# Kernel tuning notes

Measured on AMD Instinct MI355X. Metric: run time of the kernel, lower is better.

The kernel has to match this reference:

```python
import jax, jax.numpy as jnp
import numpy as np

NUM_ITERS = 3

def squash(t, axis):
    # scale = |t|^2/(1+|t|^2); out = scale * t / |t|
    sn = jnp.sum(t * t, axis=axis, keepdims=True)
    return (sn / (1.0 + sn)) * t / jnp.sqrt(sn)


def setup_inputs() -> dict:
    key = jax.random.key(0)
    k1, k2, k3, k4 = jax.random.split(key, 4)
    B = 128
    inputs = jax.random.normal(k1, (B, 256, 20, 20), dtype=jnp.float32)
    conv_w = jax.random.normal(k2, (8, 32, 256, 9, 9), dtype=jnp.float32) * 0.05
    conv_b = jax.random.normal(k3, (8, 32), dtype=jnp.float32) * 0.05
    route_weights = jax.random.normal(k4, (10, 1152, 8, 16), dtype=jnp.float32)
    return {"inputs": inputs, "conv_w": conv_w, "conv_b": conv_b,
            "route_weights": route_weights}


def reference(inputs, conv_w, conv_b, route_weights):
    B = inputs.shape[0]
    K, O, Cin, kh, kw = conv_w.shape          # 8 capsules, 32 out-chans each
    # --- primary capsules: 8 parallel convs fused into one grouped-output conv ---
    w = conv_w.reshape(K * O, Cin, kh, kw)
    out = jax.lax.conv_general_dilated(
        inputs, w, window_strides=(2, 2), padding='VALID',
        dimension_numbers=('NCHW', 'OIHW', 'NCHW'))  # [B, K*O, 6, 6]
    out = out + conv_b.reshape(K * O)[None, :, None, None]
    H = out.shape[-1]
    x = out.reshape(B, K, O * H * H).transpose(0, 2, 1)  # [B, 1152, 8]
    x = squash(x, axis=2)
    # --- routing layer ---
    # prediction_vectors: x[None,:,:,None,:] @ W[:,None,:,:,:] -> [10,B,1152,1,16]
    pred = jnp.einsum('bri,crio->cbro', x, route_weights)[:, :, :, None, :]
    logits = jnp.zeros_like(pred)
    v = None
    for i in range(NUM_ITERS):
        # routing_softmax(dim=2): softmax over the routes axis (faithful to source)
        c = jax.nn.softmax(logits, axis=2)
        s = jnp.sum(c * pred, axis=2, keepdims=True)  # [10,B,1,1,16]
        v = squash(s, axis=1)                          # squash default dim=1 (batch) -- faithful
        if i != NUM_ITERS - 1:
            logits = logits + jnp.sum(pred * v, axis=-1, keepdims=True)
    # [10,B,1,1,16] -> squeeze -> [10,B,16] -> permute(1,0,2) -> [B,10,16]
    return jnp.squeeze(v).transpose(1, 0, 2)
```

## Files before the change

kernel.cpp:

```cpp
#include <hip/hip_runtime.h>
#include <math.h>

typedef _Float16 f16;
typedef _Float16 f16x8 __attribute__((ext_vector_type(8)));
typedef float f32x4 __attribute__((ext_vector_type(4)));
typedef float f32x8 __attribute__((ext_vector_type(8)));

#define AS1 __attribute__((address_space(1)))
#define AS3 __attribute__((address_space(3)))

__device__ __forceinline__ void gld_lds16(const f16* g, f16* l) {
#if defined(__has_builtin) && __has_builtin(__builtin_amdgcn_global_load_lds)
    __builtin_amdgcn_global_load_lds((const AS1 void*)g, (AS3 void*)l, 16, 0, 0);
#else
    *(uint4*)l = *(const uint4*)g;
#endif
}

__global__ __launch_bounds__(256) void transpose_input(
    const float* __restrict__ inp, f16* __restrict__ out)
{
    const int b = blockIdx.x, c0 = blockIdx.y * 32, p0 = blockIdx.z * 32;
    const int tx = threadIdx.x, ty = threadIdx.y;
    __shared__ float t[32][33];
#pragma unroll
    for (int j = 0; j < 4; ++j) {
        int c = ty + j * 8, p = p0 + tx;
        if (p < 400) t[c][tx] = inp[((size_t)b * 256 + c0 + c) * 400 + p];
    }
    __syncthreads();
#pragma unroll
    for (int j = 0; j < 4; ++j) {
        int p = p0 + ty + j * 8;
        if (p < 400) out[((size_t)b * 400 + p) * 256 + c0 + tx] = (f16)t[tx][ty + j * 8];
    }
}

__global__ __launch_bounds__(256) void permute_w(
    const float* __restrict__ cw, f16* __restrict__ w_t)
{
    const int n = blockIdx.x, t = threadIdx.x;
    __shared__ f16 buf[81 * 258];
    const float* src = cw + (size_t)n * 20736;
    for (int i = t; i < 20736; i += 256) {
        int cin = i / 81, p = i - cin * 81;
        buf[p * 258 + cin] = (f16)src[i];
    }
    __syncthreads();
    f16* dst = w_t + (size_t)n * 20736;
    for (int j = t; j < 20736; j += 256) {
        int p = j >> 8, cin = j & 255;
        dst[j] = buf[p * 258 + cin];
    }
}

#define SPLITK 14
__global__ __launch_bounds__(256, 2) void conv_mfma(
    const f16* __restrict__ in_t,
    const f16* __restrict__ w_t,
    f16* __restrict__ part)
{
    __shared__ f16 As[3][128 * 32];
    __shared__ f16 Bs[3][256 * 32];
    const int tid = threadIdx.x;
    const int lane = tid & 63, wave = tid >> 6;
    const int wm = wave >> 1, wn = wave & 1;

    const int bid = blockIdx.x + 36 * blockIdx.z;
    const int wgid = (bid & 7) * 63 + (bid >> 3);
    const int m0 = (wgid % 36) * 128;
    const int kz = wgid / 36;

    const int kc0 = kz * 46 + (kz < 4 ? kz : 4);
    const int NT  = (kz < 4) ? 47 : 46;

    int srcA[2], srcB[4];
#pragma unroll
    for (int i = 0; i < 2; ++i) {
        int pairp = i * 32 + (tid >> 3);
        int chunk8 = (tid & 7) ^ (pairp & 7);
        int e = chunk8 >> 2, q4 = chunk8 & 3;
        int m = m0 + pairp * 2 + e;
        int b = m / 36, hw = m - b * 36;
        int ho = hw / 6, wo = hw - ho * 6;
        srcA[i] = ((b * 20 + 2 * ho) * 20 + 2 * wo) * 256 + q4 * 8;
    }
#pragma unroll
    for (int i = 0; i < 4; ++i) {
        int pairp = i * 32 + (tid >> 3);
        int chunk8 = (tid & 7) ^ (pairp & 7);
        int e = chunk8 >> 2, q4 = chunk8 & 3;
        int n = pairp * 2 + e;
        srcB[i] = n * 20736 + q4 * 8;
    }

    const int row = lane & 15, quad = lane >> 4;
    int offA[4], offB[8];
#pragma unroll
    for (int mt = 0; mt < 4; ++mt) {
        int m = wm * 64 + mt * 16 + row;
        int ph8 = (((m & 1) << 2) + quad) ^ ((m >> 1) & 7);
        offA[mt] = (m >> 1) * 64 + ph8 * 8;
    }
#pragma unroll
    for (int nt = 0; nt < 8; ++nt) {
        int n = wn * 128 + nt * 16 + row;
        int ph8 = (((n & 1) << 2) + quad) ^ ((n >> 1) & 7);
        offB[nt] = (n >> 1) * 64 + ph8 * 8;
    }

    f32x4 acc[4][8] = {};

#define STAGE(T, BUF) do {                                                    \
        int kc = kc0 + (T);                                                   \
        int p = kc >> 3, cq = kc & 7;                                         \
        int kh = p / 9, kw = p - kh * 9;                                      \
        int koffA = (kh * 20 + kw) * 256 + cq * 32;                           \
        int koffB = kc * 32;                                                  \
        _Pragma("unroll")                                                     \
        for (int i = 0; i < 2; ++i)                                           \
            gld_lds16(in_t + srcA[i] + koffA, &As[BUF][i * 2048 + tid * 8]);  \
        _Pragma("unroll")                                                     \
        for (int i = 0; i < 4; ++i)                                           \
            gld_lds16(w_t + srcB[i] + koffB, &Bs[BUF][i * 2048 + tid * 8]);   \
    } while (0)

    STAGE(0, 0);
    STAGE(1, 1);

    int buf = 0;
    for (int t = 0; t < NT; ++t) {
        if (t + 1 < NT)
            asm volatile("s_waitcnt vmcnt(6)\n\ts_barrier" ::: "memory");
        else
            asm volatile("s_waitcnt vmcnt(0)\n\ts_barrier" ::: "memory");
        if (t + 2 < NT) {
            int bn = buf + 2; if (bn >= 3) bn -= 3;
            STAGE(t + 2, bn);
        }
        const f16* Ab = &As[buf][0];
        const f16* Bb = &Bs[buf][0];
        f16x8 af[4], bfr[8];
#pragma unroll
        for (int mt = 0; mt < 4; ++mt) af[mt] = *(const f16x8*)(Ab + offA[mt]);
#pragma unroll
        for (int nt = 0; nt < 8; ++nt) bfr[nt] = *(const f16x8*)(Bb + offB[nt]);
        __builtin_amdgcn_s_setprio(1);
#pragma unroll
        for (int mt = 0; mt < 4; ++mt)
#pragma unroll
            for (int nt = 0; nt < 8; ++nt)
                acc[mt][nt] = __builtin_amdgcn_mfma_f32_16x16x32_f16(
                    af[mt], bfr[nt], acc[mt][nt], 0, 0, 0);
        __builtin_amdgcn_s_setprio(0);
        if (++buf == 3) buf = 0;
    }
#undef STAGE

    const int col = lane & 15, qr = (lane >> 4) * 4;
    f16* pb = part + (size_t)kz * 4608 * 256;
#pragma unroll
    for (int mt = 0; mt < 4; ++mt)
#pragma unroll
        for (int rg = 0; rg < 4; ++rg) {
            int m = m0 + wm * 64 + mt * 16 + qr + rg;
#pragma unroll
            for (int nt = 0; nt < 8; ++nt) {
                int n = wn * 128 + nt * 16 + col;
                pb[(size_t)m * 256 + n] = (f16)acc[mt][nt][rg];
            }
        }
}

__global__ __launch_bounds__(256) void combine_squash(
    const f16* __restrict__ part, const float* __restrict__ bias,
    float* __restrict__ x)
{
    int idx = blockIdx.x * 256 + threadIdx.x;
    int m = idx >> 5, o = idx & 31;
    int b = m / 36, hw = m - b * 36;
    float val[8];
#pragma unroll
    for (int k = 0; k < 8; ++k) val[k] = bias[k * 32 + o];
#pragma unroll
    for (int s = 0; s < SPLITK; ++s) {
        const f16* p = part + ((size_t)s * 4608 + m) * 256 + o;
#pragma unroll
        for (int k = 0; k < 8; ++k) val[k] += (float)p[k * 32];
    }
    float sn = 0.f;
#pragma unroll
    for (int k = 0; k < 8; ++k) sn += val[k] * val[k];
    float scale = sqrtf(sn) / (1.f + sn);
    int r = o * 36 + hw;
    float* xp = x + ((size_t)b * 1152 + r) * 8;
#pragma unroll
    for (int k = 0; k < 8; ++k) xp[k] = val[k] * scale;
}

__global__ __launch_bounds__(256) void pred_s0(
    const float* __restrict__ x, const float* __restrict__ rw,
    f16* __restrict__ pred, float* __restrict__ s0)
{
    const int c = blockIdx.x, r0 = blockIdx.y * 32, b0 = blockIdx.z * 32;
    const int tid = threadIdx.x;
    const int o = tid & 15, rp = tid >> 4;
    const int r = r0 + rp * 2;

    __shared__ float s_sh[32 * 16];
    s_sh[tid] = 0.f; s_sh[tid + 256] = 0.f;

    float W0[8], W1[8];
    const float* wb = rw + ((size_t)(c * 1152 + r) * 8) * 16 + o;
#pragma unroll
    for (int k = 0; k < 8; ++k) { W0[k] = wb[k * 16]; W1[k] = wb[128 + k * 16]; }
    __syncthreads();

    for (int bb = 0; bb < 32; ++bb) {
        const int b = b0 + bb;
        const float4* xp = (const float4*)(x + ((size_t)b * 1152 + r) * 8);
        float4 xa = xp[0], xb = xp[1], xc = xp[2], xd = xp[3];
        float p0 = xa.x * W0[0] + xa.y * W0[1] + xa.z * W0[2] + xa.w * W0[3]
                 + xb.x * W0[4] + xb.y * W0[5] + xb.z * W0[6] + xb.w * W0[7];
        float p1 = xc.x * W1[0] + xc.y * W1[1] + xc.z * W1[2] + xc.w * W1[3]
                 + xd.x * W1[4] + xd.y * W1[5] + xd.z * W1[6] + xd.w * W1[7];
        f16* pb = pred + ((size_t)(c * 128 + b) * 1152 + r) * 16 + o;
        pb[0]  = (f16)p0;
        pb[16] = (f16)p1;
        float ps = p0 + p1;
        ps += __shfl_xor(ps, 16);
        ps += __shfl_xor(ps, 32);
        if ((tid & 63) < 16) atomicAdd(&s_sh[bb * 16 + o], ps);
    }
    __syncthreads();
    for (int i = tid; i < 512; i += 256) {
        int bb = i >> 4, oo = i & 15;
        atomicAdd(&s0[((size_t)c * 128 + b0 + bb) * 16 + oo], s_sh[i]);
    }
}

__global__ __launch_bounds__(256) void route_f16(
    const f16* __restrict__ pred, const float* __restrict__ s_in,
    const float* __restrict__ z_in, const float* __restrict__ a_in,
    float* __restrict__ a_out, float* __restrict__ s_out, float* __restrict__ z_out)
{
    const int c = blockIdx.x, b = blockIdx.y, tid = threadIdx.x;
    const size_t base = (size_t)(c * 128 + b) * 1152;

    __shared__ float vs[16];
    __shared__ float mat[128][17];
    __shared__ float red[256][16];
    __shared__ float red2[16][16];
    __shared__ float zred[256];
    __shared__ float zpart[16];

    {
        if (tid < 128) {
            float zin = z_in ? 1.f / z_in[c * 128 + tid] : (1.f / 1152.f);
            const float* sp = s_in + (size_t)(c * 128 + tid) * 16;
#pragma unroll
            for (int o = 0; o < 16; ++o) mat[tid][o] = sp[o] * zin;
        }
        __syncthreads();
        if (tid < 16) {
            float sn = 0.f;
            for (int i = 0; i < 128; ++i) { float q = mat[i][tid]; sn += q * q; }
            vs[tid] = mat[b][tid] * sqrtf(sn) / (1.f + sn);
        }
        __syncthreads();
    }

    float sacc[16];
#pragma unroll
    for (int o = 0; o < 16; ++o) sacc[o] = 0.f;
    float zacc = 0.f;

    for (int r = tid; r < 1152; r += 256) {
        const f16x8* pp = (const f16x8*)(pred + (base + r) * 16);
        f32x8 q0 = __builtin_convertvector(pp[0], f32x8);
        f32x8 q1 = __builtin_convertvector(pp[1], f32x8);
        float contrib = 0.f;
#pragma unroll
        for (int j = 0; j < 8; ++j) contrib += q0[j] * vs[j] + q1[j] * vs[j + 8];
        float an = contrib + (a_in ? a_in[base + r] : 0.f);
        if (a_out) a_out[base + r] = an;
        float e = __expf(an);
#pragma unroll
        for (int j = 0; j < 8; ++j) { sacc[j] += e * q0[j]; sacc[j + 8] += e * q1[j]; }
        zacc += e;
    }

#pragma unroll
    for (int o = 0; o < 16; ++o) red[tid][o] = sacc[o];
    zred[tid] = zacc;
    __syncthreads();
    {
        const int o = tid & 15, seg = tid >> 4;
        float t = 0.f;
#pragma unroll
        for (int j = 0; j < 16; ++j) t += red[seg * 16 + j][o];
        red2[seg][o] = t;
        if (tid < 16) {
            float tz = 0.f;
#pragma unroll
            for (int j = 0; j < 16; ++j) tz += zred[tid * 16 + j];
            zpart[tid] = tz;
        }
    }
    __syncthreads();
    if (tid < 16) {
        float t = 0.f;
#pragma unroll
        for (int seg = 0; seg < 16; ++seg) t += red2[seg][tid];
        s_out[(size_t)(c * 128 + b) * 16 + tid] = t;
    } else if (tid == 16) {
        float tz = 0.f;
#pragma unroll
        for (int j = 0; j < 16; ++j) tz += zpart[j];
        z_out[c * 128 + b] = tz;
    }
}

__global__ __launch_bounds__(128) void squash_final(
    const float* __restrict__ s, const float* __restrict__ z,
    float* __restrict__ out)
{
    const int c = blockIdx.x, b = threadIdx.x;
    float sv[16];
    const float* sp = s + ((size_t)c * 128 + b) * 16;
    float zin = 1.f / z[c * 128 + b];
#pragma unroll
    for (int o = 0; o < 16; ++o) sv[o] = sp[o] * zin;
    __shared__ float m[16][129];
#pragma unroll
    for (int o = 0; o < 16; ++o) m[o][b] = sv[o] * sv[o];
    __syncthreads();
    __shared__ float sn[16];
    if (b < 16) {
        float t = 0.f;
        for (int i = 0; i < 128; ++i) t += m[b][i];
        sn[b] = t;
    }
    __syncthreads();
#pragma unroll
    for (int o = 0; o < 16; ++o) {
        float scale = sqrtf(sn[o]) / (1.f + sn[o]);
        out[((size_t)b * 10 + c) * 16 + o] = sv[o] * scale;
    }
}

extern "C" void kernel_launch(void* const* d_in, const int* in_sizes, int n_in,
                              void* d_out, int out_size, void* d_ws, size_t ws_size,
                              hipStream_t stream)
{
    (void)in_sizes; (void)n_in; (void)out_size; (void)ws_size;
    const float* inp = (const float*)d_in[0];
    const float* cw  = (const float*)d_in[1];
    const float* cb  = (const float*)d_in[2];
    const float* rw  = (const float*)d_in[3];
    float* out = (float*)d_out;

    char* ws = (char*)d_ws;
    f16*   part = (f16*)(ws);
    f16*   pred = (f16*)(ws);
    float* x    = (float*)(ws + 47185920);
    float* a    = (float*)(ws + 51904512);
    float* sA   = (float*)(ws + 57802752);
    float* zA   = (float*)(ws + 57884672);
    float* sB   = (float*)(ws + 57889792);
    float* zB   = (float*)(ws + 57971712);
    f16*   in_t = (f16*)(ws + 57976832);
    f16*   w_t  = (f16*)(ws + 84191232);

    transpose_input<<<dim3(128, 8, 13), dim3(32, 8), 0, stream>>>(inp, in_t);
    permute_w<<<256, 256, 0, stream>>>(cw, w_t);
    conv_mfma<<<dim3(36, 1, SPLITK), 256, 0, stream>>>(in_t, w_t, part);
    combine_squash<<<576, 256, 0, stream>>>(part, cb, x);

    hipMemsetAsync(sA, 0, 81920, stream);
    pred_s0<<<dim3(10, 36, 4), 256, 0, stream>>>(x, rw, pred, sA);

    route_f16<<<dim3(10, 128), 256, 0, stream>>>(pred, sA, nullptr, nullptr,
                                                 a, sB, zB);
    route_f16<<<dim3(10, 128), 256, 0, stream>>>(pred, sB, zB, a,
                                                 nullptr, sA, zA);
    squash_final<<<10, 128, 0, stream>>>(sA, zA, out);
}
```

Before: 250.8 us.

## Split conv GEMM main loop into two interleaved load/MFMA phases

Restructures the triple-buffered implicit-GEMM loop into two half-iterations. Each half issues part of the next-next stage's global-to-LDS loads, reads half of the B fragments, then runs half of the MFMAs, with barriers and sched_barriers fencing each phase. The goal is to interleave memory issue with matrix math more finely, in a ping-pong style, and to cut register pressure from holding all B fragments at once. The cost is more barriers per iteration, and the hand-written vmcnt waits must stay consistent with the new load split.

```diff
diff --git a/kernel.cpp b/kernel.cpp
--- a/kernel.cpp
+++ b/kernel.cpp
@@ -111,51 +111,75 @@
 
     f32x4 acc[4][8] = {};
 
-#define STAGE(T, BUF) do {                                                    \
-        int kc = kc0 + (T);                                                   \
-        int p = kc >> 3, cq = kc & 7;                                         \
-        int kh = p / 9, kw = p - kh * 9;                                      \
-        int koffA = (kh * 20 + kw) * 256 + cq * 32;                           \
-        int koffB = kc * 32;                                                  \
-        _Pragma("unroll")                                                     \
-        for (int i = 0; i < 2; ++i)                                           \
-            gld_lds16(in_t + srcA[i] + koffA, &As[BUF][i * 2048 + tid * 8]);  \
-        _Pragma("unroll")                                                     \
-        for (int i = 0; i < 4; ++i)                                           \
-            gld_lds16(w_t + srcB[i] + koffB, &Bs[BUF][i * 2048 + tid * 8]);   \
+#define KOFFS(T) int kc = kc0 + (T); int pp = kc >> 3, cq = kc & 7;           \
+    int kh = pp / 9, kw = pp - kh * 9;                                        \
+    int koffA = (kh * 20 + kw) * 256 + cq * 32; int koffB = kc * 32;
+#define STAGE1(T, BUF) do { KOFFS(T)                                          \
+        gld_lds16(in_t + srcA[0] + koffA, &As[BUF][tid * 8]);                 \
+        gld_lds16(in_t + srcA[1] + koffA, &As[BUF][2048 + tid * 8]);          \
+        gld_lds16(w_t + srcB[0] + koffB, &Bs[BUF][tid * 8]);                  \
     } while (0)
-
-    STAGE(0, 0);
-    STAGE(1, 1);
+#define STAGE2(T, BUF) do { KOFFS(T)                                          \
+        gld_lds16(w_t + srcB[1] + koffB, &Bs[BUF][2048 + tid * 8]);           \
+        gld_lds16(w_t + srcB[2] + koffB, &Bs[BUF][4096 + tid * 8]);           \
+        gld_lds16(w_t + srcB[3] + koffB, &Bs[BUF][6144 + tid * 8]);           \
+    } while (0)
+
+    STAGE1(0, 0); STAGE2(0, 0);
+    STAGE1(1, 1); STAGE2(1, 1);
+    asm volatile("s_waitcnt vmcnt(6)" ::: "memory");
+    __builtin_amdgcn_s_barrier();
 
     int buf = 0;
     for (int t = 0; t < NT; ++t) {
-        if (t + 1 < NT)
-            asm volatile("s_waitcnt vmcnt(6)\n\ts_barrier" ::: "memory");
-        else
-            asm volatile("s_waitcnt vmcnt(0)\n\ts_barrier" ::: "memory");
-        if (t + 2 < NT) {
-            int bn = buf + 2; if (bn >= 3) bn -= 3;
-            STAGE(t + 2, bn);
-        }
         const f16* Ab = &As[buf][0];
         const f16* Bb = &Bs[buf][0];
+        int bn = buf + 2; if (bn >= 3) bn -= 3;
         f16x8 af[4], bfr[8];
+
 #pragma unroll
         for (int mt = 0; mt < 4; ++mt) af[mt] = *(const f16x8*)(Ab + offA[mt]);
 #pragma unroll
-        for (int nt = 0; nt < 8; ++nt) bfr[nt] = *(const f16x8*)(Bb + offB[nt]);
+        for (int nt = 0; nt < 4; ++nt) bfr[nt] = *(const f16x8*)(Bb + offB[nt]);
+        if (t + 2 < NT) STAGE1(t + 2, bn);
+        __builtin_amdgcn_s_barrier();
+        asm volatile("s_waitcnt lgkmcnt(0)" ::: "memory");
+        __builtin_amdgcn_sched_barrier(0);
         __builtin_amdgcn_s_setprio(1);
 #pragma unroll
         for (int mt = 0; mt < 4; ++mt)
 #pragma unroll
-            for (int nt = 0; nt < 8; ++nt)
+            for (int nt = 0; nt < 4; ++nt)
                 acc[mt][nt] = __builtin_amdgcn_mfma_f32_16x16x32_f16(
                     af[mt], bfr[nt], acc[mt][nt], 0, 0, 0);
         __builtin_amdgcn_s_setprio(0);
+        __builtin_amdgcn_s_barrier();
+
+#pragma unroll
+        for (int nt = 4; nt < 8; ++nt) bfr[nt] = *(const f16x8*)(Bb + offB[nt]);
+        if (t + 2 < NT) STAGE2(t + 2, bn);
+        if (t + 2 < NT)
+            asm volatile("s_waitcnt vmcnt(6)" ::: "memory");
+        else if (t + 1 < NT)
+            asm volatile("s_waitcnt vmcnt(0)" ::: "memory");
+        __builtin_amdgcn_s_barrier();
+        asm volatile("s_waitcnt lgkmcnt(0)" ::: "memory");
+        __builtin_amdgcn_sched_barrier(0);
+        __builtin_amdgcn_s_setprio(1);
+#pragma unroll
+        for (int mt = 0; mt < 4; ++mt)
+#pragma unroll
+            for (int nt = 4; nt < 8; ++nt)
+                acc[mt][nt] = __builtin_amdgcn_mfma_f32_16x16x32_f16(
+                    af[mt], bfr[nt], acc[mt][nt], 0, 0, 0);
+        __builtin_amdgcn_s_setprio(0);
+        __builtin_amdgcn_s_barrier();
+
         if (++buf == 3) buf = 0;
     }
-#undef STAGE
+#undef STAGE1
+#undef STAGE2
+#undef KOFFS
 
     const int col = lane & 15, qr = (lane >> 4) * 4;
     f16* pb = part + (size_t)kz * 4608 * 256;
```

After: 246.1 us. About the same (-1.9%).
